# Performance work log

Hardware: AMD Instinct MI355X
Metric: run time of the kernel (lower is better)

Reference implementation:

```python
import jax, jax.numpy as jnp
import numpy as np

FIR_LEN = 8192  # fsm_fir_len


def setup_inputs() -> dict:
    key = jax.random.key(0)
    k1, k2, k3, k4 = jax.random.split(key, 4)
    B, C, L, K = 8, 2, 524288, 6
    return {
        "input_signal": jax.random.normal(k1, (B, C, L), dtype=jnp.float32),
        "Bs": jax.random.normal(k2, (B, K, 3), dtype=jnp.float32),
        "A1_pre": jax.random.normal(k3, (B, K), dtype=jnp.float32),
        "A2_pre": jax.random.normal(k4, (B, K), dtype=jnp.float32),
    }


def reference(input_signal, Bs, A1_pre, A2_pre):
    # Stability-enforcing activations for the feedback coefficients
    A1 = 2.0 * jnp.tanh(A1_pre)                               # [B, K]
    A1_abs = jnp.abs(A1)
    A2 = ((2.0 - A1_abs) * jnp.tanh(A2_pre) + A1_abs) / 2.0   # [B, K]
    As = jnp.stack([jnp.ones_like(A1), A1, A2], axis=-1)      # [B, K, 3]

    # Frequency-sampling method: sample DTFT of each biquad on FIR_LEN DFT bins
    Bf = jnp.fft.rfft(Bs, n=FIR_LEN, axis=-1)                 # [B, K, F]
    Af = jnp.fft.rfft(As, n=FIR_LEN, axis=-1)                 # [B, K, F]
    H = jnp.prod(Bf / Af, axis=1)                             # [B, F] cascade of K biquads

    # FIR approximation of the IIR via inverse DFT
    fir = jnp.fft.irfft(H, n=FIR_LEN, axis=-1)                # [B, FIR_LEN]

    # Causal FFT convolution with the input signal, truncated to length L
    L = input_signal.shape[-1]
    conv_len = L + FIR_LEN - 1
    X = jnp.fft.rfft(input_signal, n=conv_len, axis=-1)       # [B, C, Fc]
    Hc = jnp.fft.rfft(fir, n=conv_len, axis=-1)               # [B, Fc]
    y = jnp.fft.irfft(X * Hc[:, None, :], n=conv_len, axis=-1)[..., :L]
    return y.astype(input_signal.dtype)
```

## Files before the change

### kernel.cpp

```cpp
#include <hip/hip_runtime.h>

#define FIR_LEN 8192
#define NFREQ   4097
#define L_SIG   524288
#define NB      8
#define NC      2
#define NK      6
#define TWO_PI  6.283185307179586f

typedef __attribute__((ext_vector_type(8))) short bf16x8;
typedef __attribute__((ext_vector_type(4))) float f32x4;

__device__ inline short f2bf(float f) {
  union { float f; unsigned u; } v; v.f = f;
  unsigned u = v.u;
  unsigned r = (u + 0x7fffu + ((u >> 16) & 1u)) >> 16;
  return (short)r;
}

__global__ void k_freqresp(const float* __restrict__ Bs,
                           const float* __restrict__ A1p,
                           const float* __restrict__ A2p,
                           float2* __restrict__ H) {
  __shared__ float sb0[NK], sb1[NK], sb2[NK], sa1[NK], sa2[NK];
  const int b = blockIdx.x, tid = threadIdx.x;
  if (tid < NK) {
    sb0[tid] = Bs[(b*NK+tid)*3+0];
    sb1[tid] = Bs[(b*NK+tid)*3+1];
    sb2[tid] = Bs[(b*NK+tid)*3+2];
    float a1 = 2.0f * tanhf(A1p[b*NK+tid]);
    float aa = fabsf(a1);
    sa1[tid] = a1;
    sa2[tid] = ((2.0f - aa) * tanhf(A2p[b*NK+tid]) + aa) * 0.5f;
  }
  __syncthreads();
  for (int f = tid; f < NFREQ; f += blockDim.x) {
    float th = (float)f * (TWO_PI / FIR_LEN);
    float s1, c1;
    sincosf(th, &s1, &c1);
    float c2 = c1*c1 - s1*s1, s2 = 2.0f*s1*c1;
    float hr = 1.0f, hi = 0.0f;
#pragma unroll
    for (int k = 0; k < NK; ++k) {
      float nr = sb0[k] + sb1[k]*c1 + sb2[k]*c2;
      float ni = -(sb1[k]*s1 + sb2[k]*s2);
      float dr = 1.0f + sa1[k]*c1 + sa2[k]*c2;
      float di = -(sa1[k]*s1 + sa2[k]*s2);
      float inv = 1.0f / (dr*dr + di*di);
      float rr = (nr*dr + ni*di) * inv;
      float ri = (ni*dr - nr*di) * inv;
      float t  = hr*rr - hi*ri;
      hi = hr*ri + hi*rr;
      hr = t;
    }
    H[b*NFREQ+f] = make_float2(hr, hi);
  }
}

__global__ __launch_bounds__(256) void k_ifft_s1(const float2* __restrict__ H,
                                                 float2* __restrict__ G) {
  __shared__ float2 tw[64];
  const int tid = threadIdx.x;
  if (tid < 64) {
    float s, c;
    sincosf((float)tid * (TWO_PI / 64.0f), &s, &c);
    tw[tid] = make_float2(c, s);
  }
  __syncthreads();
  const int b = blockIdx.x >> 5;
  const int f1 = (blockIdx.x & 31) * 4 + (tid >> 6);
  const int r = tid & 63;
  const float2* Hb = H + b * NFREQ;

  float Gr = 0.f, Gi = 0.f;
#pragma unroll 4
  for (int f2 = 0; f2 < 64; ++f2) {
    int f = 128 * f2 + f1;
    int neg = f > 4096;
    int fi = neg ? 8192 - f : f;
    float2 h = Hb[fi];
    float hi = neg ? -h.y : h.y;
    float2 w = tw[(f2 * r) & 63];
    Gr = fmaf(h.x, w.x, Gr); Gr = fmaf(-hi, w.y, Gr);
    Gi = fmaf(h.x, w.y, Gi); Gi = fmaf( hi, w.x, Gi);
  }
  G[(b * 128 + f1) * 64 + r] = make_float2(Gr, Gi);
}

__global__ __launch_bounds__(256) void k_ifft_s2(const float2* __restrict__ G,
                                                 float* __restrict__ fir) {
  __shared__ float2 Gs[8192];
  const int b = blockIdx.x >> 5, nblk = blockIdx.x & 31, tid = threadIdx.x;
  for (int i = tid; i < 8192; i += 256) Gs[i] = G[b * 8192 + i];
  __syncthreads();

  const int n = nblk * 256 + tid;
  const int r = n & 63;
  float sd, cd;
  sincosf((float)n * (TWO_PI / FIR_LEN), &sd, &cd);
  float c[4], s[4], acc[4] = {0.f, 0.f, 0.f, 0.f};
#pragma unroll
  for (int q = 0; q < 4; ++q) {
    float ph = (float)((n * (32 * q)) & (FIR_LEN - 1)) * (TWO_PI / FIR_LEN);
    sincosf(ph, &s[q], &c[q]);
  }
#pragma unroll 4
  for (int mm = 0; mm < 32; ++mm) {
#pragma unroll
    for (int q = 0; q < 4; ++q) {
      float2 g = Gs[((q * 32 + mm) << 6) + r];
      acc[q] = fmaf(g.x, c[q], acc[q]);
      acc[q] = fmaf(-g.y, s[q], acc[q]);
      float t = fmaf(c[q], cd, -(s[q] * sd));
      s[q]    = fmaf(s[q], cd,   c[q] * sd);
      c[q] = t;
    }
  }
  fir[b * FIR_LEN + n] = (acc[0] + acc[1] + acc[2] + acc[3]) * (1.0f / FIR_LEN);
}

#define GTOP 8719
#define GN   8736
__global__ void k_packA(const float* __restrict__ fir, short* __restrict__ Gc) {
  const int b = blockIdx.x >> 3, p = blockIdx.x & 7;
  short* g = Gc + ((size_t)(b*8 + p)) * GN;
  for (int v = threadIdx.x; v < GN; v += 256) {
    int fidx = GTOP - v - p;
    float f = (fidx >= 0 && fidx < FIR_LEN) ? fir[b*FIR_LEN + fidx] : 0.0f;
    g[v] = f2bf(f);
  }
}

#define HPAD   8208
#define WROWS  32768
#define WN     (HPAD + WROWS)
#define LXS    42264
#define NSTEP  256

#define MFMA16(a,bb,c) __builtin_amdgcn_mfma_f32_16x16x32_bf16(a,bb,c,0,0,0)
#define BADDR(r) (2*(r) + (((r) >> 8) << 4))

__global__ __launch_bounds__(512, 2) void k_conv_mfma(
    const float* __restrict__ x, const short* __restrict__ Gc,
    float* __restrict__ y) {
  __shared__ short xs[LXS];
  const int tid = threadIdx.x;
  const int bc = blockIdx.x >> 4, tileIdx = blockIdx.x & 15;
  const int b = bc >> 1;
  const long base = (long)bc * L_SIG;
  const int t0 = tileIdx * WROWS;

  const float* xg = x + base + t0 - HPAD;
  for (int k = tid * 4; k < WN; k += 2048) {
    int g = t0 - HPAD + k;
    float4 v;
    if (g >= 0) {
      v = *(const float4*)(xg + k);
    } else if (g <= -4) {
      v = make_float4(0.f, 0.f, 0.f, 0.f);
    } else {
      v.x = (g + 0 >= 0) ? xg[k + 0] : 0.f;
      v.y = (g + 1 >= 0) ? xg[k + 1] : 0.f;
      v.z = (g + 2 >= 0) ? xg[k + 2] : 0.f;
      v.w = (g + 3 >= 0) ? xg[k + 3] : 0.f;
    }
    int o = k + ((k >> 8) << 3);
    short4 s4 = make_short4(f2bf(v.x), f2bf(v.y), f2bf(v.z), f2bf(v.w));
    *(short4*)(xs + o) = s4;
  }

  const int wv = tid >> 6, l = tid & 63;
  const int nl = l & 15, h = l >> 4, dl = h >> 1, j0 = (h & 1) * 8;
  const int In = 16 * wv + nl;

  const int A0 = GTOP - nl + j0;
  const int p = A0 & 7;
  const short* ap = Gc + ((size_t)b * 8 + p) * GN + (A0 - p) - 16 * dl;

  f32x4 acc[16];
  const f32x4 z4 = {0.f, 0.f, 0.f, 0.f};
#pragma unroll
  for (int m = 0; m < 16; ++m) acc[m] = z4;

  __syncthreads();

  const char* xsb = (const char*)xs;
  int rb = HPAD + 256 * In + j0 - 16 * dl;
  bf16x8 bw[16];
#pragma unroll
  for (int m = 0; m < 16; ++m) {
    int r0 = rb + 16 * m;
    bw[m] = *(const bf16x8*)(xsb + BADDR(r0));
  }

  bf16x8 aF = *(const bf16x8*)(ap);
  const short* apn = ap - 32;

  for (int s8 = 0; s8 < NSTEP / 8; ++s8) {
#pragma unroll
    for (int u = 0; u < 8; ++u) {
      acc[14] = MFMA16(aF, bw[(14 - 2*u) & 15], acc[14]);
      acc[15] = MFMA16(aF, bw[(15 - 2*u) & 15], acc[15]);
      rb -= 32;
      bw[(14 - 2*u) & 15] = *(const bf16x8*)(xsb + BADDR(rb));
      bw[(15 - 2*u) & 15] = *(const bf16x8*)(xsb + BADDR(rb + 16));
      bf16x8 aN = *(const bf16x8*)(apn);
      apn -= 32;
#pragma unroll
      for (int m = 0; m < 14; ++m)
        acc[m] = MFMA16(aF, bw[(m - 2*u) & 15], acc[m]);
      aF = aN;
    }
  }
#pragma unroll
  for (int m = 0; m < 16; ++m) acc[m] = MFMA16(aF, bw[m], acc[m]);

  float* yo = y + base + t0;
#pragma unroll
  for (int m = 0; m < 16; ++m)
    *(f32x4*)(yo + 256 * In + 16 * m + 4 * h) = acc[m];
}

extern "C" void kernel_launch(void* const* d_in, const int* in_sizes, int n_in,
                              void* d_out, int out_size, void* d_ws, size_t ws_size,
                              hipStream_t stream) {
  const float* x   = (const float*)d_in[0];
  const float* Bs  = (const float*)d_in[1];
  const float* A1p = (const float*)d_in[2];
  const float* A2p = (const float*)d_in[3];
  float* y = (float*)d_out;

  float*  wsf = (float*)d_ws;
  float2* H   = (float2*)wsf;
  float*  fir = wsf + 65552;
  short*  Gc  = (short*)(wsf + 131088);
  float2* G   = (float2*)(wsf + 410640);

  k_freqresp<<<NB, 256, 0, stream>>>(Bs, A1p, A2p, H);
  k_ifft_s1<<<NB * 32, 256, 0, stream>>>(H, G);
  k_ifft_s2<<<NB * 32, 256, 0, stream>>>(G, fir);
  k_packA<<<NB * 8, 256, 0, stream>>>(fir, Gc);
  k_conv_mfma<<<NB * NC * (L_SIG / WROWS), 512, 0, stream>>>(x, Gc, y);
}
```

Measured before the change: 205.0 us.

## Fuse FIR-design kernels and halve conv tile for higher occupancy

```diff
diff --git a/kernel.cpp b/kernel.cpp
--- a/kernel.cpp
+++ b/kernel.cpp
@@ -18,12 +18,17 @@
   return (short)r;
 }
 
-__global__ void k_freqresp(const float* __restrict__ Bs,
-                           const float* __restrict__ A1p,
-                           const float* __restrict__ A2p,
-                           float2* __restrict__ H) {
+__global__ __launch_bounds__(256) void k_ifft_s1(const float* __restrict__ Bs,
+                                                 const float* __restrict__ A1p,
+                                                 const float* __restrict__ A2p,
+                                                 float2* __restrict__ G) {
   __shared__ float sb0[NK], sb1[NK], sb2[NK], sa1[NK], sa2[NK];
-  const int b = blockIdx.x, tid = threadIdx.x;
+  __shared__ float2 Hs[256];
+  __shared__ float2 tw[64];
+  const int tid = threadIdx.x;
+  const int b = blockIdx.x >> 5;
+  const int f1base = (blockIdx.x & 31) * 4;
+
   if (tid < NK) {
     sb0[tid] = Bs[(b*NK+tid)*3+0];
     sb1[tid] = Bs[(b*NK+tid)*3+1];
@@ -33,8 +38,16 @@
     sa1[tid] = a1;
     sa2[tid] = ((2.0f - aa) * tanhf(A2p[b*NK+tid]) + aa) * 0.5f;
   }
-  __syncthreads();
-  for (int f = tid; f < NFREQ; f += blockDim.x) {
+  if (tid < 64) {
+    float s, c;
+    sincosf((float)tid * (TWO_PI / 64.0f), &s, &c);
+    tw[tid] = make_float2(c, s);
+  }
+  __syncthreads();
+
+  {
+    const int f1l = tid >> 6, f2 = tid & 63;
+    const int f = 128 * f2 + f1base + f1l;
     float th = (float)f * (TWO_PI / FIR_LEN);
     float s1, c1;
     sincosf(th, &s1, &c1);
@@ -53,45 +66,29 @@
       hi = hr*ri + hi*rr;
       hr = t;
     }
-    H[b*NFREQ+f] = make_float2(hr, hi);
-  }
-}
-
-__global__ __launch_bounds__(256) void k_ifft_s1(const float2* __restrict__ H,
-                                                 float2* __restrict__ G) {
-  __shared__ float2 tw[64];
-  const int tid = threadIdx.x;
-  if (tid < 64) {
-    float s, c;
-    sincosf((float)tid * (TWO_PI / 64.0f), &s, &c);
-    tw[tid] = make_float2(c, s);
-  }
-  __syncthreads();
-  const int b = blockIdx.x >> 5;
-  const int f1 = (blockIdx.x & 31) * 4 + (tid >> 6);
-  const int r = tid & 63;
-  const float2* Hb = H + b * NFREQ;
-
+    Hs[tid] = make_float2(hr, hi);
+  }
+  __syncthreads();
+
+  const int f1l = tid >> 6, r = tid & 63;
   float Gr = 0.f, Gi = 0.f;
 #pragma unroll 4
   for (int f2 = 0; f2 < 64; ++f2) {
-    int f = 128 * f2 + f1;
-    int neg = f > 4096;
-    int fi = neg ? 8192 - f : f;
-    float2 h = Hb[fi];
-    float hi = neg ? -h.y : h.y;
+    float2 h = Hs[64 * f1l + f2];
     float2 w = tw[(f2 * r) & 63];
-    Gr = fmaf(h.x, w.x, Gr); Gr = fmaf(-hi, w.y, Gr);
-    Gi = fmaf(h.x, w.y, Gi); Gi = fmaf( hi, w.x, Gi);
-  }
-  G[(b * 128 + f1) * 64 + r] = make_float2(Gr, Gi);
-}
-
+    Gr = fmaf(h.x, w.x, Gr); Gr = fmaf(-h.y, w.y, Gr);
+    Gi = fmaf(h.x, w.y, Gi); Gi = fmaf( h.y, w.x, Gi);
+  }
+  G[((size_t)b * 128 + f1base + f1l) * 64 + r] = make_float2(Gr, Gi);
+}
+
+#define GTOP 8719
+#define GN   8736
 __global__ __launch_bounds__(256) void k_ifft_s2(const float2* __restrict__ G,
-                                                 float* __restrict__ fir) {
+                                                 short* __restrict__ Gc) {
   __shared__ float2 Gs[8192];
   const int b = blockIdx.x >> 5, nblk = blockIdx.x & 31, tid = threadIdx.x;
-  for (int i = tid; i < 8192; i += 256) Gs[i] = G[b * 8192 + i];
+  for (int i = tid; i < 8192; i += 256) Gs[i] = G[(size_t)b * 8192 + i];
   __syncthreads();
 
   const int n = nblk * 256 + tid;
@@ -116,36 +113,36 @@
       c[q] = t;
     }
   }
-  fir[b * FIR_LEN + n] = (acc[0] + acc[1] + acc[2] + acc[3]) * (1.0f / FIR_LEN);
-}
-
-#define GTOP 8719
-#define GN   8736
-__global__ void k_packA(const float* __restrict__ fir, short* __restrict__ Gc) {
-  const int b = blockIdx.x >> 3, p = blockIdx.x & 7;
-  short* g = Gc + ((size_t)(b*8 + p)) * GN;
-  for (int v = threadIdx.x; v < GN; v += 256) {
-    int fidx = GTOP - v - p;
-    float f = (fidx >= 0 && fidx < FIR_LEN) ? fir[b*FIR_LEN + fidx] : 0.0f;
-    g[v] = f2bf(f);
+  const short bv = f2bf((acc[0] + acc[1] + acc[2] + acc[3]) * (1.0f / FIR_LEN));
+  short* gb = Gc + (size_t)b * 8 * GN;
+#pragma unroll
+  for (int p = 0; p < 8; ++p)
+    gb[p * GN + (GTOP - n - p)] = bv;
+
+  if (nblk == 0) {
+#pragma unroll
+    for (int p = 0; p < 8; ++p) {
+      for (int v = tid; v < 528 - p; v += 256) gb[p * GN + v] = 0;
+      if (tid < 16 + p) gb[p * GN + 8720 - p + tid] = 0;
+    }
   }
 }
 
 #define HPAD   8208
-#define WROWS  32768
+#define WROWS  16384
 #define WN     (HPAD + WROWS)
-#define LXS    42264
+#define LXS    25368
 #define NSTEP  256
 
 #define MFMA16(a,bb,c) __builtin_amdgcn_mfma_f32_16x16x32_bf16(a,bb,c,0,0,0)
 #define BADDR(r) (2*(r) + (((r) >> 8) << 4))
 
-__global__ __launch_bounds__(512, 2) void k_conv_mfma(
+__global__ __launch_bounds__(512, 4) void k_conv_mfma(
     const float* __restrict__ x, const short* __restrict__ Gc,
     float* __restrict__ y) {
   __shared__ short xs[LXS];
   const int tid = threadIdx.x;
-  const int bc = blockIdx.x >> 4, tileIdx = blockIdx.x & 15;
+  const int bc = blockIdx.x >> 5, tileIdx = blockIdx.x & 31;
   const int b = bc >> 1;
   const long base = (long)bc * L_SIG;
   const int t0 = tileIdx * WROWS;
@@ -171,54 +168,57 @@
 
   const int wv = tid >> 6, l = tid & 63;
   const int nl = l & 15, h = l >> 4, dl = h >> 1, j0 = (h & 1) * 8;
-  const int In = 16 * wv + nl;
+  const int In = 16 * (wv & 3) + nl;
+  const int mbase = 8 * (wv >> 2);
 
   const int A0 = GTOP - nl + j0;
   const int p = A0 & 7;
   const short* ap = Gc + ((size_t)b * 8 + p) * GN + (A0 - p) - 16 * dl;
 
-  f32x4 acc[16];
+  f32x4 acc[8];
   const f32x4 z4 = {0.f, 0.f, 0.f, 0.f};
 #pragma unroll
-  for (int m = 0; m < 16; ++m) acc[m] = z4;
+  for (int mm = 0; mm < 8; ++mm) acc[mm] = z4;
+
+  bf16x8 aF = *(const bf16x8*)(ap);
+  bf16x8 aN = *(const bf16x8*)(ap - 32);
+  const short* apn = ap - 64;
 
   __syncthreads();
 
   const char* xsb = (const char*)xs;
-  int rb = HPAD + 256 * In + j0 - 16 * dl;
-  bf16x8 bw[16];
-#pragma unroll
-  for (int m = 0; m < 16; ++m) {
-    int r0 = rb + 16 * m;
-    bw[m] = *(const bf16x8*)(xsb + BADDR(r0));
-  }
-
-  bf16x8 aF = *(const bf16x8*)(ap);
-  const short* apn = ap - 32;
-
-  for (int s8 = 0; s8 < NSTEP / 8; ++s8) {
-#pragma unroll
-    for (int u = 0; u < 8; ++u) {
-      acc[14] = MFMA16(aF, bw[(14 - 2*u) & 15], acc[14]);
-      acc[15] = MFMA16(aF, bw[(15 - 2*u) & 15], acc[15]);
+  int rb = HPAD + 256 * In + 16 * mbase + j0 - 16 * dl;
+  bf16x8 bw[8];
+#pragma unroll
+  for (int mm = 0; mm < 8; ++mm) {
+    int r0 = rb + 16 * mm;
+    bw[mm] = *(const bf16x8*)(xsb + BADDR(r0));
+  }
+
+  for (int s4i = 0; s4i < NSTEP / 4; ++s4i) {
+#pragma unroll
+    for (int u = 0; u < 4; ++u) {
+      acc[6] = MFMA16(aF, bw[(6 - 2*u) & 7], acc[6]);
+      acc[7] = MFMA16(aF, bw[(7 - 2*u) & 7], acc[7]);
       rb -= 32;
-      bw[(14 - 2*u) & 15] = *(const bf16x8*)(xsb + BADDR(rb));
-      bw[(15 - 2*u) & 15] = *(const bf16x8*)(xsb + BADDR(rb + 16));
-      bf16x8 aN = *(const bf16x8*)(apn);
+      bw[(6 - 2*u) & 7] = *(const bf16x8*)(xsb + BADDR(rb));
+      bw[(7 - 2*u) & 7] = *(const bf16x8*)(xsb + BADDR(rb + 16));
+      bf16x8 aN2 = *(const bf16x8*)(apn);
       apn -= 32;
 #pragma unroll
-      for (int m = 0; m < 14; ++m)
-        acc[m] = MFMA16(aF, bw[(m - 2*u) & 15], acc[m]);
+      for (int mm = 0; mm < 6; ++mm)
+        acc[mm] = MFMA16(aF, bw[(mm - 2*u) & 7], acc[mm]);
       aF = aN;
-    }
-  }
-#pragma unroll
-  for (int m = 0; m < 16; ++m) acc[m] = MFMA16(aF, bw[m], acc[m]);
+      aN = aN2;
+    }
+  }
+#pragma unroll
+  for (int mm = 0; mm < 8; ++mm) acc[mm] = MFMA16(aF, bw[mm], acc[mm]);
 
   float* yo = y + base + t0;
 #pragma unroll
-  for (int m = 0; m < 16; ++m)
-    *(f32x4*)(yo + 256 * In + 16 * m + 4 * h) = acc[m];
+  for (int mm = 0; mm < 8; ++mm)
+    *(f32x4*)(yo + 256 * In + 16 * (mbase + mm) + 4 * h) = acc[mm];
 }
 
 extern "C" void kernel_launch(void* const* d_in, const int* in_sizes, int n_in,
@@ -230,15 +230,10 @@
   const float* A2p = (const float*)d_in[3];
   float* y = (float*)d_out;
 
-  float*  wsf = (float*)d_ws;
-  float2* H   = (float2*)wsf;
-  float*  fir = wsf + 65552;
-  short*  Gc  = (short*)(wsf + 131088);
-  float2* G   = (float2*)(wsf + 410640);
-
-  k_freqresp<<<NB, 256, 0, stream>>>(Bs, A1p, A2p, H);
-  k_ifft_s1<<<NB * 32, 256, 0, stream>>>(H, G);
-  k_ifft_s2<<<NB * 32, 256, 0, stream>>>(G, fir);
-  k_packA<<<NB * 8, 256, 0, stream>>>(fir, Gc);
+  short*  Gc = (short*)d_ws;
+  float2* G  = (float2*)((char*)d_ws + (size_t)NB*8*GN*2);
+
+  k_ifft_s1<<<NB * 32, 256, 0, stream>>>(Bs, A1p, A2p, G);
+  k_ifft_s2<<<NB * 32, 256, 0, stream>>>(G, Gc);
   k_conv_mfma<<<NB * NC * (L_SIG / WROWS), 512, 0, stream>>>(x, Gc, y);
 }
```

Measured after the change: 193.5 us. 1.06x faster.
